# Kernel optimization log

Measured on AMD Instinct MI355X. Metric: run time of the kernel, lower is better.

## Reference

```python
import jax, jax.numpy as jnp
import numpy as np

NUM_HEADS = 12
HEAD_DIM = 64
HIDDEN = NUM_HEADS * HEAD_DIM
SCALE = 1.0 / float(np.sqrt(HEAD_DIM))


def _split_heads(x):
    # x: [b, d, s, hidden] -> [b, h, d, s, head_dim]  (transpose_for_scores)
    b, d, s, _ = x.shape
    return jnp.transpose(x.reshape(b, d, s, NUM_HEADS, HEAD_DIM), (0, 3, 1, 2, 4))


def _merge_heads(x):
    # [b, h, d, s, e] -> [b, d, s, hidden]  (untranspose_for_scores)
    b, h, d, s, e = x.shape
    return jnp.transpose(x, (0, 2, 3, 1, 4)).reshape(b, d, s, h * e)


def _segment_attention(q, keys, values, masks, num_docs):
    # _cat_forward: broadcast every key/value/mask list entry to num_docs along
    # dim 2, concat along key length, then scaled-dot-product attention.
    b, h = q.shape[0], q.shape[1]
    q = jnp.broadcast_to(q, (b, h, num_docs, q.shape[3], q.shape[4]))
    k = jnp.concatenate([jnp.broadcast_to(t, (b, h, num_docs, t.shape[3], t.shape[4])) for t in keys], axis=3)
    v = jnp.concatenate([jnp.broadcast_to(t, (b, h, num_docs, t.shape[3], t.shape[4])) for t in values], axis=3)
    mask = jnp.concatenate([jnp.broadcast_to(m, (b, 1, num_docs, 1, m.shape[-1])) for m in masks], axis=-1)
    scores = jnp.einsum('bhdqe,bhdke->bhdqk', q, k) * SCALE + mask
    probs = jax.nn.softmax(scores, axis=-1)
    ctx = jnp.einsum('bhdqk,bhdke->bhdqe', probs, v)
    return _merge_heads(ctx)


def setup_inputs() -> dict:
    key = jax.random.key(0)
    ks = jax.random.split(key, 8)
    B, D, Q, S = 2, 16, 32, 512
    inp = {
        'cls': jax.random.normal(ks[0], (B, 1, 1, HIDDEN), jnp.float32),
        'query': jax.random.normal(ks[1], (B, 1, Q, HIDDEN), jnp.float32),
        'doc': jax.random.normal(ks[2], (B, D, S, HIDDEN), jnp.float32),
        'qmask': jnp.zeros((B, 1, 1, 1, Q), jnp.float32),
        'dmask': jnp.zeros((B, 1, D, 1, S), jnp.float32),
        'Wq': jax.random.normal(ks[3], (HIDDEN, HIDDEN), jnp.float32) * 0.02,
        'bq': jnp.zeros((HIDDEN,), jnp.float32),
        'Wk': jax.random.normal(ks[4], (HIDDEN, HIDDEN), jnp.float32) * 0.02,
        'bk': jnp.zeros((HIDDEN,), jnp.float32),
        'Wv': jax.random.normal(ks[5], (HIDDEN, HIDDEN), jnp.float32) * 0.02,
        'bv': jnp.zeros((HIDDEN,), jnp.float32),
    }
    return inp


def reference(cls, query, doc, qmask, dmask, Wq, bq, Wk, bk, Wv, bv):
    num_docs = doc.shape[1]
    b = cls.shape[0]
    # per-segment q/k/v projections + head split
    segs = {}
    for name, hs in (('cls', cls), ('query', query), ('doc', doc)):
        segs[name] = tuple(_split_heads(hs @ W.T + bb) for W, bb in ((Wq, bq), (Wk, bk), (Wv, bv)))
    cmask = jnp.zeros((b, 1, 1, 1, cls.shape[2]), cls.dtype)  # cls token never padded
    masks = {'cls': cmask, 'query': qmask, 'doc': dmask}
    names = ('cls', 'query', 'doc')
    keys = [segs[n][1] for n in names]
    vals = [segs[n][2] for n in names]
    mlist = [masks[n] for n in names]
    # all segment->segment attention flags default True; attention_window_size
    # is None so each segment goes through the _cat_forward path
    outs = [_segment_attention(segs[n][0], keys, vals, mlist, num_docs) for n in names]
    # cls:[b,D,1,H], query:[b,D,Q,H], doc:[b,D,S,H] -> concat along seq for one output
    return jnp.concatenate(outs, axis=2)
```

## Files before the change

kernel.cpp:

```cpp
#include <hip/hip_runtime.h>
#include <hip/hip_bf16.h>

#define NH      12
#define HD      64
#define HID     768
#define B_      2
#define D_      16
#define QL      32
#define SL      512
#define SEQ     545
#define RPB     8225
#define TOT_ROWS 16450
#define PAD_ROWS 16512
#define VT_R    8256
#define WSZ     589824
#define SCALE_  0.125f
#define LOG2E   1.4426950408889634f
#define QSF     0.18033688011112042f

typedef __attribute__((ext_vector_type(8))) short short8;
typedef __attribute__((ext_vector_type(4))) short short4v;
typedef __attribute__((ext_vector_type(4))) float float4v;
typedef __attribute__((ext_vector_type(2))) unsigned int uint2v;

__device__ __forceinline__ short f2bf(float f) {
    __hip_bfloat16 h = __float2bfloat16(f);
    short s; __builtin_memcpy(&s, &h, 2);
    return s;
}

__device__ __forceinline__ unsigned int cvtpk(float a, float b) {
    unsigned int r;
    asm("v_cvt_pk_bf16_f32 %0, %1, %2" : "=v"(r) : "v"(a), "v"(b));
    return r;
}

__device__ __forceinline__ void gl2lds16(const short* g, short* l) {
    __builtin_amdgcn_global_load_lds(
        (const __attribute__((address_space(1))) void*)g,
        (__attribute__((address_space(3))) void*)l, 16, 0, 0);
}

#define PACK_BLKS  12384
#define WPACK_BLKS 1728

__global__ __launch_bounds__(256) void pack_all(
    const float* __restrict__ cls, const float* __restrict__ query,
    const float* __restrict__ doc,
    const float* __restrict__ Wq, const float* __restrict__ Wk,
    const float* __restrict__ Wv,
    short* __restrict__ X, short* __restrict__ Wb)
{
    int bid = blockIdx.x;
    if (bid < PACK_BLKS) {
        int idx = (bid * 256 + threadIdx.x) * 4;
        int row = idx / HID;
        int col = idx - row * HID;
        float4 v = make_float4(0.f, 0.f, 0.f, 0.f);
        if (row < TOT_ROWS) {
            int b = row / RPB;
            int r = row - b * RPB;
            const float* src;
            if (r == 0)        src = cls   + b * HID + col;
            else if (r < 33)   src = query + ((size_t)(b * QL + (r - 1))) * HID + col;
            else               src = doc   + ((size_t)(b * (D_ * SL) + (r - 33))) * HID + col;
            v = *reinterpret_cast<const float4*>(src);
        }
        short4v o;
        o[0] = f2bf(v.x); o[1] = f2bf(v.y); o[2] = f2bf(v.z); o[3] = f2bf(v.w);
        *reinterpret_cast<short4v*>(X + idx) = o;
    } else {
        int idx = ((bid - PACK_BLKS) * 256 + threadIdx.x) * 4;
        int z = idx / WSZ;
        int r = idx - z * WSZ;
        const float* src = (z == 0 ? Wq : (z == 1 ? Wk : Wv)) + r;
        float sc = (z == 0) ? QSF : 1.0f;
        float4 v = *reinterpret_cast<const float4*>(src);
        short4v o;
        o[0] = f2bf(v.x * sc); o[1] = f2bf(v.y * sc);
        o[2] = f2bf(v.z * sc); o[3] = f2bf(v.w * sc);
        *reinterpret_cast<short4v*>(Wb + idx) = o;
    }
}

__global__ __launch_bounds__(256) void proj4u(
    const short* __restrict__ X, const short* __restrict__ Wb,
    const float* __restrict__ bq, const float* __restrict__ bk,
    const float* __restrict__ bv,
    short* __restrict__ Qb, short* __restrict__ Kb, short* __restrict__ Vt)
{
    __shared__ short Xs[2][128 * 64];
    __shared__ short Ws[2][128 * 64];

    int tid = threadIdx.x, lane = tid & 63, wave = tid >> 6;

    int lin = blockIdx.x + 18 * blockIdx.y;
    {
        const int q = 290, r = 2;
        int xcd = lin & 7, seq = lin >> 3;
        lin = (xcd < r ? xcd * (q + 1) : r * (q + 1) + (xcd - r) * q) + seq;
    }
    int mblk = lin / 18;
    int nz   = lin - mblk * 18;
    int zi   = nz % 3;
    int nblk = nz / 3;
    bool vsw = (zi == 2);
    const short* W = Wb + (size_t)zi * WSZ;
    int m0 = mblk * 128, n0 = nblk * 128;

    int moff = (wave & 1) * 64, noff = (wave >> 1) * 64;
    int lr = lane & 15, lg = lane >> 4;

    const short* xsrc[4];
    const short* wsrc[4];
#pragma unroll
    for (int p = 0; p < 4; ++p) {
        int s = p * 256 + tid;
        int row = s >> 3, c = s & 7;
        int col = (c ^ (row & 7)) * 8;
        xsrc[p] = X + (size_t)(m0 + row) * HID + col;
        wsrc[p] = W + (size_t)(n0 + row) * HID + col;
    }

    float4v acc[4][4];
    for (int mi = 0; mi < 4; ++mi)
        for (int ni = 0; ni < 4; ++ni)
            acc[mi][ni] = (float4v){0.f, 0.f, 0.f, 0.f};

#define PSTAGE(bufi, kt) do {                                               \
    _Pragma("unroll")                                                       \
    for (int p = 0; p < 4; ++p) {                                           \
        gl2lds16(xsrc[p] + (kt) * 64,                                       \
                 &Xs[bufi][(p * 256 + (tid & 0xC0)) * 8]);                  \
        gl2lds16(wsrc[p] + (kt) * 64,                                       \
                 &Ws[bufi][(p * 256 + (tid & 0xC0)) * 8]);                  \
    } } while (0)

    PSTAGE(0, 0);
#pragma unroll
    for (int kt = 0; kt < 12; ++kt) {
        __syncthreads();
        if (kt < 11) PSTAGE((kt + 1) & 1, kt + 1);
        const short* xb = Xs[kt & 1];
        const short* wb = Ws[kt & 1];
        short8 afl[4], afh[4], bfl[4], bfh[4];
        for (int mi = 0; mi < 4; ++mi) {
            int r = moff + mi * 16 + lr;
            int x0 = lg ^ (r & 7);
            afl[mi] = *reinterpret_cast<const short8*>(&xb[r * 64 + x0 * 8]);
            afh[mi] = *reinterpret_cast<const short8*>(&xb[r * 64 + (x0 ^ 4) * 8]);
        }
        for (int ni = 0; ni < 4; ++ni) {
            int r = noff + ni * 16 + lr;
            int x0 = lg ^ (r & 7);
            bfl[ni] = *reinterpret_cast<const short8*>(&wb[r * 64 + x0 * 8]);
            bfh[ni] = *reinterpret_cast<const short8*>(&wb[r * 64 + (x0 ^ 4) * 8]);
        }
        if (!vsw) {
            for (int mi = 0; mi < 4; ++mi)
                for (int ni = 0; ni < 4; ++ni) {
                    acc[mi][ni] = __builtin_amdgcn_mfma_f32_16x16x32_bf16(
                        afl[mi], bfl[ni], acc[mi][ni], 0, 0, 0);
                    acc[mi][ni] = __builtin_amdgcn_mfma_f32_16x16x32_bf16(
                        afh[mi], bfh[ni], acc[mi][ni], 0, 0, 0);
                }
        } else {
            for (int mi = 0; mi < 4; ++mi)
                for (int ni = 0; ni < 4; ++ni) {
                    acc[mi][ni] = __builtin_amdgcn_mfma_f32_16x16x32_bf16(
                        bfl[ni], afl[mi], acc[mi][ni], 0, 0, 0);
                    acc[mi][ni] = __builtin_amdgcn_mfma_f32_16x16x32_bf16(
                        bfh[ni], afh[mi], acc[mi][ni], 0, 0, 0);
                }
        }
    }
#undef PSTAGE

    if (!vsw) {
        short* Y = zi == 0 ? Qb : Kb;
        const float* bias = zi == 0 ? bq : bk;
        float bsc = zi == 0 ? QSF : 1.0f;
        for (int ni = 0; ni < 4; ++ni) {
            int gcol = n0 + noff + ni * 16 + lr;
            float bb = bias[gcol] * bsc;
            for (int mi = 0; mi < 4; ++mi) {
                int growb = m0 + moff + mi * 16 + lg * 4;
                for (int r = 0; r < 4; ++r)
                    Y[(size_t)(growb + r) * HID + gcol] = f2bf(acc[mi][ni][r] + bb);
            }
        }
    } else {
        for (int ni = 0; ni < 4; ++ni) {
            float4 b4 = *reinterpret_cast<const float4*>(&bv[n0 + noff + ni * 16 + lg * 4]);
            const float* bbr = reinterpret_cast<const float*>(&b4);
            for (int mi = 0; mi < 4; ++mi) {
                int grow = m0 + moff + mi * 16 + lr;
                if (grow >= TOT_ROWS) continue;
                int b  = grow >= RPB ? 1 : 0;
                int rb = grow - b * RPB;
                int vr = rb < 33 ? rb : rb + 7;
                size_t cb = ((size_t)(b * HID + n0 + noff + ni * 16 + lg * 4)) * VT_R;
                for (int r = 0; r < 4; ++r)
                    Vt[cb + (size_t)r * VT_R + vr] = f2bf(acc[mi][ni][r] + bbr[r]);
            }
        }
    }
}

__global__ __launch_bounds__(256) void attn5(
    const short* __restrict__ Qb, const short* __restrict__ Kb,
    const short* __restrict__ Vt,
    const float* __restrict__ qmask, const float* __restrict__ dmask,
    float* __restrict__ out)
{
    __shared__ short Ks[3][64 * 64];
    __shared__ short Vs[3][64 * 64];
    __shared__ float maskv[576];

    int tid  = threadIdx.x;
    int lane = tid & 63, wave = tid >> 6;

    int lin = blockIdx.x + 3 * blockIdx.y;
    {
        int xcd = lin & 7, seq = lin >> 3;
        lin = xcd * 144 + seq;
    }
    int hbd = lin / 3;
    int qc  = lin - hbd * 3;
    int h = hbd >> 5, bd = hbd & 31;
    int b = bd >> 4, d = bd & 15;

    int lr = lane & 15, lg = lane >> 4, lk = lg * 8;
    int base = b * RPB;
    const short* vbase = Vt + (size_t)(b * HID + h * HD) * VT_R;

    const short* kp[2]; const short* vp[2];
    const short* kp8[2]; const short* vp8[2];
    int loff[2];
#pragma unroll
    for (int p = 0; p < 2; ++p) {
        int s2 = p * 256 + tid;
        int r = s2 >> 3, c = s2 & 7;
        int colsw = (c ^ (r & 7)) * 8;
        kp[p] = Kb + (size_t)(base + 33 + d * SL + r) * HID + h * HD + colsw;
        vp[p] = vbase + (size_t)r * VT_R + 40 + d * SL + colsw;
        int r8 = r > 32 ? 32 : r;
        kp8[p] = Kb + (size_t)(base + r8) * HID + h * HD + colsw;
        vp8[p] = vbase + (size_t)r * VT_R + colsw;
        loff[p] = (p * 256 + (tid & 0xC0)) * 8;
    }

#define ALIN(bufi, kt) do {                                       \
    gl2lds16(kp[0] + (size_t)(kt) * 64 * HID, &Ks[bufi][loff[0]]);\
    gl2lds16(kp[1] + (size_t)(kt) * 64 * HID, &Ks[bufi][loff[1]]);\
    gl2lds16(vp[0] + (kt) * 64, &Vs[bufi][loff[0]]);              \
    gl2lds16(vp[1] + (kt) * 64, &Vs[bufi][loff[1]]); } while (0)
#define A8(bufi) do {                                             \
    gl2lds16(kp8[0], &Ks[bufi][loff[0]]);                         \
    gl2lds16(kp8[1], &Ks[bufi][loff[1]]);                         \
    gl2lds16(vp8[0], &Vs[bufi][loff[0]]);                         \
    gl2lds16(vp8[1], &Vs[bufi][loff[1]]); } while (0)

    ALIN(0, 0);
    ALIN(1, 1);

    for (int i = tid; i < 576; i += 256) {
        float mv;
        if (i < 512)       mv = dmask[(size_t)(b * D_ + d) * SL + i];
        else if (i == 512) mv = 0.f;
        else if (i < 545)  mv = qmask[b * QL + (i - 513)];
        else               mv = -INFINITY;
        maskv[i] = mv * LOG2E;
    }

    short8 bq0[3], bq1[3];
#pragma unroll
    for (int s = 0; s < 3; ++s) {
        int qtok = qc * 192 + s * 64 + wave * 16 + lr;
        int qrow = qtok < 512 ? base + 33 + d * SL + qtok : base + qtok - 512;
        const short* qp = Qb + (size_t)qrow * HID + h * HD + lk;
        bq0[s] = *reinterpret_cast<const short8*>(qp);
        bq1[s] = *reinterpret_cast<const short8*>(qp + 32);
    }

    float m_i[3] = {-1e30f, -1e30f, -1e30f};
    float lp[3]  = {0.f, 0.f, 0.f};
    float4v o[3][4];
    for (int s = 0; s < 3; ++s)
        for (int nt = 0; nt < 4; ++nt) o[s][nt] = (float4v){0.f, 0.f, 0.f, 0.f};

    __syncthreads();

#pragma unroll
    for (int kt = 0; kt < 9; ++kt) {
        if (kt >= 1) {
            if (kt == 8) { asm volatile("s_waitcnt vmcnt(0)" ::: "memory"); }
            else         { asm volatile("s_waitcnt vmcnt(4)" ::: "memory"); }
            __builtin_amdgcn_s_barrier();
            __builtin_amdgcn_sched_barrier(0);
        }
        if (kt < 6)       ALIN((kt + 2) % 3, kt + 2);
        else if (kt == 6) A8((kt + 2) % 3);

        const short* kb   = Ks[kt % 3];
        const short* vbuf = Vs[kt % 3];

        float4v mk[4];
        short8 kf0[4], kf1[4];
#pragma unroll
        for (int nt = 0; nt < 4; ++nt) {
            mk[nt] = *reinterpret_cast<const float4v*>(
                &maskv[kt * 64 + nt * 16 + lg * 4]);
            int r = nt * 16 + lr;
            int x0 = lg ^ (r & 7);
            kf0[nt] = *reinterpret_cast<const short8*>(&kb[r * 64 + x0 * 8]);
            kf1[nt] = *reinterpret_cast<const short8*>(&kb[r * 64 + (x0 ^ 4) * 8]);
        }

#pragma unroll
        for (int s = 0; s < 3; ++s) {
            float p4[4][4];
            __builtin_amdgcn_s_setprio(1);
            for (int nt = 0; nt < 4; ++nt) {
                float4v z = mk[nt];
                z = __builtin_amdgcn_mfma_f32_16x16x32_bf16(kf0[nt], bq0[s], z, 0, 0, 0);
                z = __builtin_amdgcn_mfma_f32_16x16x32_bf16(kf1[nt], bq1[s], z, 0, 0, 0);
                for (int r = 0; r < 4; ++r) p4[nt][r] = z[r];
            }
            __builtin_amdgcn_s_setprio(0);

            float c0 = fmaxf(fmaxf(p4[0][0], p4[0][1]), p4[0][2]);
            float c1 = fmaxf(fmaxf(p4[0][3], p4[1][0]), p4[1][1]);
            float c2 = fmaxf(fmaxf(p4[1][2], p4[1][3]), p4[2][0]);
            float c3 = fmaxf(fmaxf(p4[2][1], p4[2][2]), p4[2][3]);
            float c4 = fmaxf(fmaxf(p4[3][0], p4[3][1]), p4[3][2]);
            float lmax = fmaxf(fmaxf(fmaxf(c0, c1), fmaxf(c2, c3)),
                               fmaxf(c4, p4[3][3]));

            if (__any(lmax > m_i[s] + 8.0f)) {
                float tmx = fmaxf(lmax, __shfl_xor(lmax, 16));
                tmx = fmaxf(tmx, __shfl_xor(tmx, 32));
                float mnew = fmaxf(m_i[s], tmx);
                float alpha = exp2f(m_i[s] - mnew);
                m_i[s] = mnew;
                lp[s] *= alpha;
                float al[4];
                for (int r = 0; r < 4; ++r) al[r] = __shfl(alpha, lg * 4 + r);
                for (int nt = 0; nt < 4; ++nt)
                    for (int r = 0; r < 4; ++r) o[s][nt][r] *= al[r];
            }

            for (int nt = 0; nt < 4; ++nt)
                for (int r = 0; r < 4; ++r)
                    p4[nt][r] = exp2f(p4[nt][r] - m_i[s]);
            float s0 = (p4[0][0] + p4[0][1]) + (p4[0][2] + p4[0][3]);
            float s1 = (p4[1][0] + p4[1][1]) + (p4[1][2] + p4[1][3]);
            float s2 = (p4[2][0] + p4[2][1]) + (p4[2][2] + p4[2][3]);
            float s3 = (p4[3][0] + p4[3][1]) + (p4[3][2] + p4[3][3]);
            lp[s] += (s0 + s1) + (s2 + s3);

            unsigned int wa[4], wbv[4];
            for (int nt = 0; nt < 4; ++nt) {
                wa[nt]  = cvtpk(p4[nt][0], p4[nt][1]);
                wbv[nt] = cvtpk(p4[nt][2], p4[nt][3]);
            }
            uint2v tA01 = __builtin_amdgcn_permlane32_swap(wa[0],  wa[1],  false, false);
            uint2v uA01 = __builtin_amdgcn_permlane16_swap(tA01[0], tA01[1], false, false);
            uint2v tB01 = __builtin_amdgcn_permlane32_swap(wbv[0], wbv[1], false, false);
            uint2v uB01 = __builtin_amdgcn_permlane16_swap(tB01[0], tB01[1], false, false);
            uint2v tA23 = __builtin_amdgcn_permlane32_swap(wa[2],  wa[3],  false, false);
            uint2v uA23 = __builtin_amdgcn_permlane16_swap(tA23[0], tA23[1], false, false);
            uint2v tB23 = __builtin_amdgcn_permlane32_swap(wbv[2], wbv[3], false, false);
            uint2v uB23 = __builtin_amdgcn_permlane16_swap(tB23[0], tB23[1], false, false);

            union { unsigned int u[4]; short8 s8; } A0, A1;
            A0.u[0] = uA01[0]; A0.u[1] = uB01[0]; A0.u[2] = uA01[1]; A0.u[3] = uB01[1];
            A1.u[0] = uA23[0]; A1.u[1] = uB23[0]; A1.u[2] = uA23[1]; A1.u[3] = uB23[1];
            short8 ap0 = A0.s8;
            short8 ap1 = A1.s8;

            __builtin_amdgcn_s_setprio(1);
            for (int nt = 0; nt < 4; ++nt) {
                int rd = nt * 16 + lr;
                int x0 = lg ^ (rd & 7);
                short8 bv0 = *reinterpret_cast<const short8*>(&vbuf[rd * 64 + x0 * 8]);
                short8 bv1 = *reinterpret_cast<const short8*>(&vbuf[rd * 64 + (x0 ^ 4) * 8]);
                o[s][nt] = __builtin_amdgcn_mfma_f32_16x16x32_bf16(ap0, bv0, o[s][nt], 0, 0, 0);
                o[s][nt] = __builtin_amdgcn_mfma_f32_16x16x32_bf16(ap1, bv1, o[s][nt], 0, 0, 0);
            }
            __builtin_amdgcn_s_setprio(0);
        }
    }
#undef ALIN
#undef A8

    for (int s = 0; s < 3; ++s) {
        float lt = lp[s];
        lt += __shfl_xor(lt, 16);
        lt += __shfl_xor(lt, 32);
        float li[4];
        for (int r = 0; r < 4; ++r) li[r] = __shfl(lt, lg * 4 + r);
        for (int r = 0; r < 4; ++r) {
            int t = qc * 192 + s * 64 + wave * 16 + lg * 4 + r;
            if (t >= SEQ) continue;
            int seq = t < 512 ? 33 + t : (t == 512 ? 0 : t - 512);
            float inv = 1.f / li[r];
            float* op = out + ((size_t)(bd * SEQ + seq)) * HID + h * HD + lr;
            for (int nt = 0; nt < 4; ++nt)
                op[nt * 16] = o[s][nt][r] * inv;
        }
    }
}

extern "C" void kernel_launch(void* const* d_in, const int* in_sizes, int n_in,
                              void* d_out, int out_size, void* d_ws, size_t ws_size,
                              hipStream_t stream)
{
    const float* cls   = (const float*)d_in[0];
    const float* query = (const float*)d_in[1];
    const float* doc   = (const float*)d_in[2];
    const float* qmask = (const float*)d_in[3];
    const float* dmask = (const float*)d_in[4];
    const float* Wq = (const float*)d_in[5];
    const float* bq = (const float*)d_in[6];
    const float* Wk = (const float*)d_in[7];
    const float* bk = (const float*)d_in[8];
    const float* Wv = (const float*)d_in[9];
    const float* bv = (const float*)d_in[10];
    float* out = (float*)d_out;

    short* X  = (short*)d_ws;
    size_t seg = (size_t)PAD_ROWS * HID;
    short* Qb = X + seg;
    short* Kb = Qb + seg;
    short* Vt = Kb + seg;
    short* Wb = (short*)d_out;

    pack_all<<<dim3(PACK_BLKS + WPACK_BLKS), 256, 0, stream>>>(
        cls, query, doc, Wq, Wk, Wv, X, Wb);
    proj4u<<<dim3(18, 129, 1), 256, 0, stream>>>(X, Wb, bq, bk, bv, Qb, Kb, Vt);
    attn5<<<dim3(3, NH * 32, 1), 256, 0, stream>>>(Qb, Kb, Vt, qmask, dmask, out);
}
```

Baseline: 278.3 us.

## Split attention query sub-tiles across 12 waves instead of looping in 4

```diff
diff --git a/kernel.cpp b/kernel.cpp
--- a/kernel.cpp
+++ b/kernel.cpp
@@ -207,7 +207,7 @@
     }
 }
 
-__global__ __launch_bounds__(256) void attn5(
+__global__ __launch_bounds__(768) void attn6(
     const short* __restrict__ Qb, const short* __restrict__ Kb,
     const short* __restrict__ Vt,
     const float* __restrict__ qmask, const float* __restrict__ dmask,
@@ -231,40 +231,37 @@
     int b = bd >> 4, d = bd & 15;
 
     int lr = lane & 15, lg = lane >> 4, lk = lg * 8;
+    int sidx = wave >> 2, wq = wave & 3;
     int base = b * RPB;
     const short* vbase = Vt + (size_t)(b * HID + h * HD) * VT_R;
 
-    const short* kp[2]; const short* vp[2];
-    const short* kp8[2]; const short* vp8[2];
-    int loff[2];
-#pragma unroll
-    for (int p = 0; p < 2; ++p) {
-        int s2 = p * 256 + tid;
-        int r = s2 >> 3, c = s2 & 7;
+    bool stg = tid < 512;
+    int loffK = (tid & 0x1C0) * 8;
+    const short *kp = Kb, *vp = Vt, *kp8 = Kb, *vp8 = Vt;
+    {
+        int r = tid >> 3, c = tid & 7;
         int colsw = (c ^ (r & 7)) * 8;
-        kp[p] = Kb + (size_t)(base + 33 + d * SL + r) * HID + h * HD + colsw;
-        vp[p] = vbase + (size_t)r * VT_R + 40 + d * SL + colsw;
-        int r8 = r > 32 ? 32 : r;
-        kp8[p] = Kb + (size_t)(base + r8) * HID + h * HD + colsw;
-        vp8[p] = vbase + (size_t)r * VT_R + colsw;
-        loff[p] = (p * 256 + (tid & 0xC0)) * 8;
-    }
-
-#define ALIN(bufi, kt) do {                                       \
-    gl2lds16(kp[0] + (size_t)(kt) * 64 * HID, &Ks[bufi][loff[0]]);\
-    gl2lds16(kp[1] + (size_t)(kt) * 64 * HID, &Ks[bufi][loff[1]]);\
-    gl2lds16(vp[0] + (kt) * 64, &Vs[bufi][loff[0]]);              \
-    gl2lds16(vp[1] + (kt) * 64, &Vs[bufi][loff[1]]); } while (0)
-#define A8(bufi) do {                                             \
-    gl2lds16(kp8[0], &Ks[bufi][loff[0]]);                         \
-    gl2lds16(kp8[1], &Ks[bufi][loff[1]]);                         \
-    gl2lds16(vp8[0], &Vs[bufi][loff[0]]);                         \
-    gl2lds16(vp8[1], &Vs[bufi][loff[1]]); } while (0)
+        if (stg) {
+            kp  = Kb + (size_t)(base + 33 + d * SL + r) * HID + h * HD + colsw;
+            vp  = vbase + (size_t)r * VT_R + 40 + d * SL + colsw;
+            int r8 = r > 32 ? 32 : r;
+            kp8 = Kb + (size_t)(base + r8) * HID + h * HD + colsw;
+            vp8 = vbase + (size_t)r * VT_R + colsw;
+        }
+    }
+
+#define ALIN(bufi, kt) do { if (stg) {                            \
+    gl2lds16(kp + (size_t)(kt) * 64 * HID, &Ks[bufi][loffK]);     \
+    gl2lds16(vp + (kt) * 64, &Vs[bufi][loffK]); } } while (0)
+#define A8(bufi) do { if (stg) {                                  \
+    gl2lds16(kp8, &Ks[bufi][loffK]);                              \
+    gl2lds16(vp8, &Vs[bufi][loffK]); } } while (0)
 
     ALIN(0, 0);
     ALIN(1, 1);
 
-    for (int i = tid; i < 576; i += 256) {
+    if (tid < 576) {
+        int i = tid;
         float mv;
         if (i < 512)       mv = dmask[(size_t)(b * D_ + d) * SL + i];
         else if (i == 512) mv = 0.f;
@@ -273,21 +270,19 @@
         maskv[i] = mv * LOG2E;
     }
 
-    short8 bq0[3], bq1[3];
-#pragma unroll
-    for (int s = 0; s < 3; ++s) {
-        int qtok = qc * 192 + s * 64 + wave * 16 + lr;
+    short8 bq0, bq1;
+    {
+        int qtok = qc * 192 + sidx * 64 + wq * 16 + lr;
         int qrow = qtok < 512 ? base + 33 + d * SL + qtok : base + qtok - 512;
         const short* qp = Qb + (size_t)qrow * HID + h * HD + lk;
-        bq0[s] = *reinterpret_cast<const short8*>(qp);
-        bq1[s] = *reinterpret_cast<const short8*>(qp + 32);
-    }
-
-    float m_i[3] = {-1e30f, -1e30f, -1e30f};
-    float lp[3]  = {0.f, 0.f, 0.f};
-    float4v o[3][4];
-    for (int s = 0; s < 3; ++s)
-        for (int nt = 0; nt < 4; ++nt) o[s][nt] = (float4v){0.f, 0.f, 0.f, 0.f};
+        bq0 = *reinterpret_cast<const short8*>(qp);
+        bq1 = *reinterpret_cast<const short8*>(qp + 32);
+    }
+
+    float m_i = -1e30f;
+    float lp  = 0.f;
+    float4v o[4];
+    for (int nt = 0; nt < 4; ++nt) o[nt] = (float4v){0.f, 0.f, 0.f, 0.f};
 
     __syncthreads();
 
@@ -295,7 +290,7 @@
     for (int kt = 0; kt < 9; ++kt) {
         if (kt >= 1) {
             if (kt == 8) { asm volatile("s_waitcnt vmcnt(0)" ::: "memory"); }
-            else         { asm volatile("s_waitcnt vmcnt(4)" ::: "memory"); }
+            else         { asm volatile("s_waitcnt vmcnt(2)" ::: "memory"); }
             __builtin_amdgcn_s_barrier();
             __builtin_amdgcn_sched_barrier(0);
         }
@@ -305,109 +300,105 @@
         const short* kb   = Ks[kt % 3];
         const short* vbuf = Vs[kt % 3];
 
-        float4v mk[4];
+        float p4[4][4];
         short8 kf0[4], kf1[4];
 #pragma unroll
         for (int nt = 0; nt < 4; ++nt) {
-            mk[nt] = *reinterpret_cast<const float4v*>(
-                &maskv[kt * 64 + nt * 16 + lg * 4]);
             int r = nt * 16 + lr;
             int x0 = lg ^ (r & 7);
             kf0[nt] = *reinterpret_cast<const short8*>(&kb[r * 64 + x0 * 8]);
             kf1[nt] = *reinterpret_cast<const short8*>(&kb[r * 64 + (x0 ^ 4) * 8]);
         }
-
-#pragma unroll
-        for (int s = 0; s < 3; ++s) {
-            float p4[4][4];
-            __builtin_amdgcn_s_setprio(1);
-            for (int nt = 0; nt < 4; ++nt) {
-                float4v z = mk[nt];
-                z = __builtin_amdgcn_mfma_f32_16x16x32_bf16(kf0[nt], bq0[s], z, 0, 0, 0);
-                z = __builtin_amdgcn_mfma_f32_16x16x32_bf16(kf1[nt], bq1[s], z, 0, 0, 0);
-                for (int r = 0; r < 4; ++r) p4[nt][r] = z[r];
-            }
-            __builtin_amdgcn_s_setprio(0);
-
-            float c0 = fmaxf(fmaxf(p4[0][0], p4[0][1]), p4[0][2]);
-            float c1 = fmaxf(fmaxf(p4[0][3], p4[1][0]), p4[1][1]);
-            float c2 = fmaxf(fmaxf(p4[1][2], p4[1][3]), p4[2][0]);
-            float c3 = fmaxf(fmaxf(p4[2][1], p4[2][2]), p4[2][3]);
-            float c4 = fmaxf(fmaxf(p4[3][0], p4[3][1]), p4[3][2]);
-            float lmax = fmaxf(fmaxf(fmaxf(c0, c1), fmaxf(c2, c3)),
-                               fmaxf(c4, p4[3][3]));
-
-            if (__any(lmax > m_i[s] + 8.0f)) {
-                float tmx = fmaxf(lmax, __shfl_xor(lmax, 16));
-                tmx = fmaxf(tmx, __shfl_xor(tmx, 32));
-                float mnew = fmaxf(m_i[s], tmx);
-                float alpha = exp2f(m_i[s] - mnew);
-                m_i[s] = mnew;
-                lp[s] *= alpha;
-                float al[4];
-                for (int r = 0; r < 4; ++r) al[r] = __shfl(alpha, lg * 4 + r);
-                for (int nt = 0; nt < 4; ++nt)
-                    for (int r = 0; r < 4; ++r) o[s][nt][r] *= al[r];
-            }
-
+        __builtin_amdgcn_s_setprio(1);
+#pragma unroll
+        for (int nt = 0; nt < 4; ++nt) {
+            float4v z = *reinterpret_cast<const float4v*>(
+                &maskv[kt * 64 + nt * 16 + lg * 4]);
+            z = __builtin_amdgcn_mfma_f32_16x16x32_bf16(kf0[nt], bq0, z, 0, 0, 0);
+            z = __builtin_amdgcn_mfma_f32_16x16x32_bf16(kf1[nt], bq1, z, 0, 0, 0);
+            for (int r = 0; r < 4; ++r) p4[nt][r] = z[r];
+        }
+        __builtin_amdgcn_s_setprio(0);
+
+        float c0 = fmaxf(fmaxf(p4[0][0], p4[0][1]), p4[0][2]);
+        float c1 = fmaxf(fmaxf(p4[0][3], p4[1][0]), p4[1][1]);
+        float c2 = fmaxf(fmaxf(p4[1][2], p4[1][3]), p4[2][0]);
+        float c3 = fmaxf(fmaxf(p4[2][1], p4[2][2]), p4[2][3]);
+        float c4 = fmaxf(fmaxf(p4[3][0], p4[3][1]), p4[3][2]);
+        float lmax = fmaxf(fmaxf(fmaxf(c0, c1), fmaxf(c2, c3)),
+                           fmaxf(c4, p4[3][3]));
+
+        if (__any(lmax > m_i + 8.0f)) {
+            float tmx = fmaxf(lmax, __shfl_xor(lmax, 16));
+            tmx = fmaxf(tmx, __shfl_xor(tmx, 32));
+            float mnew = fmaxf(m_i, tmx);
+            float alpha = exp2f(m_i - mnew);
+            m_i = mnew;
+            lp *= alpha;
+            float al[4];
+            for (int r = 0; r < 4; ++r) al[r] = __shfl(alpha, lg * 4 + r);
             for (int nt = 0; nt < 4; ++nt)
-                for (int r = 0; r < 4; ++r)
-                    p4[nt][r] = exp2f(p4[nt][r] - m_i[s]);
-            float s0 = (p4[0][0] + p4[0][1]) + (p4[0][2] + p4[0][3]);
-            float s1 = (p4[1][0] + p4[1][1]) + (p4[1][2] + p4[1][3]);
-            float s2 = (p4[2][0] + p4[2][1]) + (p4[2][2] + p4[2][3]);
-            float s3 = (p4[3][0] + p4[3][1]) + (p4[3][2] + p4[3][3]);
-            lp[s] += (s0 + s1) + (s2 + s3);
-
-            unsigned int wa[4], wbv[4];
-            for (int nt = 0; nt < 4; ++nt) {
-                wa[nt]  = cvtpk(p4[nt][0], p4[nt][1]);
-                wbv[nt] = cvtpk(p4[nt][2], p4[nt][3]);
-            }
-            uint2v tA01 = __builtin_amdgcn_permlane32_swap(wa[0],  wa[1],  false, false);
-            uint2v uA01 = __builtin_amdgcn_permlane16_swap(tA01[0], tA01[1], false, false);
-            uint2v tB01 = __builtin_amdgcn_permlane32_swap(wbv[0], wbv[1], false, false);
-            uint2v uB01 = __builtin_amdgcn_permlane16_swap(tB01[0], tB01[1], false, false);
-            uint2v tA23 = __builtin_amdgcn_permlane32_swap(wa[2],  wa[3],  false, false);
-            uint2v uA23 = __builtin_amdgcn_permlane16_swap(tA23[0], tA23[1], false, false);
-            uint2v tB23 = __builtin_amdgcn_permlane32_swap(wbv[2], wbv[3], false, false);
-            uint2v uB23 = __builtin_amdgcn_permlane16_swap(tB23[0], tB23[1], false, false);
-
-            union { unsigned int u[4]; short8 s8; } A0, A1;
-            A0.u[0] = uA01[0]; A0.u[1] = uB01[0]; A0.u[2] = uA01[1]; A0.u[3] = uB01[1];
-            A1.u[0] = uA23[0]; A1.u[1] = uB23[0]; A1.u[2] = uA23[1]; A1.u[3] = uB23[1];
-            short8 ap0 = A0.s8;
-            short8 ap1 = A1.s8;
-
-            __builtin_amdgcn_s_setprio(1);
-            for (int nt = 0; nt < 4; ++nt) {
-                int rd = nt * 16 + lr;
-                int x0 = lg ^ (rd & 7);
-                short8 bv0 = *reinterpret_cast<const short8*>(&vbuf[rd * 64 + x0 * 8]);
-                short8 bv1 = *reinterpret_cast<const short8*>(&vbuf[rd * 64 + (x0 ^ 4) * 8]);
-                o[s][nt] = __builtin_amdgcn_mfma_f32_16x16x32_bf16(ap0, bv0, o[s][nt], 0, 0, 0);
-                o[s][nt] = __builtin_amdgcn_mfma_f32_16x16x32_bf16(ap1, bv1, o[s][nt], 0, 0, 0);
-            }
-            __builtin_amdgcn_s_setprio(0);
-        }
+                for (int r = 0; r < 4; ++r) o[nt][r] *= al[r];
+        }
+
+        for (int nt = 0; nt < 4; ++nt)
+            for (int r = 0; r < 4; ++r)
+                p4[nt][r] = exp2f(p4[nt][r] - m_i);
+        float s0 = (p4[0][0] + p4[0][1]) + (p4[0][2] + p4[0][3]);
+        float s1 = (p4[1][0] + p4[1][1]) + (p4[1][2] + p4[1][3]);
+        float s2 = (p4[2][0] + p4[2][1]) + (p4[2][2] + p4[2][3]);
+        float s3 = (p4[3][0] + p4[3][1]) + (p4[3][2] + p4[3][3]);
+        lp += (s0 + s1) + (s2 + s3);
+
+        unsigned int wa[4], wbv[4];
+        for (int nt = 0; nt < 4; ++nt) {
+            wa[nt]  = cvtpk(p4[nt][0], p4[nt][1]);
+            wbv[nt] = cvtpk(p4[nt][2], p4[nt][3]);
+        }
+        uint2v tA01 = __builtin_amdgcn_permlane32_swap(wa[0],  wa[1],  false, false);
+        uint2v uA01 = __builtin_amdgcn_permlane16_swap(tA01[0], tA01[1], false, false);
+        uint2v tB01 = __builtin_amdgcn_permlane32_swap(wbv[0], wbv[1], false, false);
+        uint2v uB01 = __builtin_amdgcn_permlane16_swap(tB01[0], tB01[1], false, false);
+        uint2v tA23 = __builtin_amdgcn_permlane32_swap(wa[2],  wa[3],  false, false);
+        uint2v uA23 = __builtin_amdgcn_permlane16_swap(tA23[0], tA23[1], false, false);
+        uint2v tB23 = __builtin_amdgcn_permlane32_swap(wbv[2], wbv[3], false, false);
+        uint2v uB23 = __builtin_amdgcn_permlane16_swap(tB23[0], tB23[1], false, false);
+
+        union { unsigned int u[4]; short8 s8; } A0, A1;
+        A0.u[0] = uA01[0]; A0.u[1] = uB01[0]; A0.u[2] = uA01[1]; A0.u[3] = uB01[1];
+        A1.u[0] = uA23[0]; A1.u[1] = uB23[0]; A1.u[2] = uA23[1]; A1.u[3] = uB23[1];
+        short8 ap0 = A0.s8;
+        short8 ap1 = A1.s8;
+
+        __builtin_amdgcn_s_setprio(1);
+#pragma unroll
+        for (int nt = 0; nt < 4; ++nt) {
+            int rd = nt * 16 + lr;
+            int x0 = lg ^ (rd & 7);
+            short8 bv0 = *reinterpret_cast<const short8*>(&vbuf[rd * 64 + x0 * 8]);
+            short8 bv1 = *reinterpret_cast<const short8*>(&vbuf[rd * 64 + (x0 ^ 4) * 8]);
+            o[nt] = __builtin_amdgcn_mfma_f32_16x16x32_bf16(ap0, bv0, o[nt], 0, 0, 0);
+            o[nt] = __builtin_amdgcn_mfma_f32_16x16x32_bf16(ap1, bv1, o[nt], 0, 0, 0);
+        }
+        __builtin_amdgcn_s_setprio(0);
     }
 #undef ALIN
 #undef A8
 
-    for (int s = 0; s < 3; ++s) {
-        float lt = lp[s];
+    {
+        float lt = lp;
         lt += __shfl_xor(lt, 16);
         lt += __shfl_xor(lt, 32);
         float li[4];
         for (int r = 0; r < 4; ++r) li[r] = __shfl(lt, lg * 4 + r);
         for (int r = 0; r < 4; ++r) {
-            int t = qc * 192 + s * 64 + wave * 16 + lg * 4 + r;
+            int t = qc * 192 + sidx * 64 + wq * 16 + lg * 4 + r;
             if (t >= SEQ) continue;
             int seq = t < 512 ? 33 + t : (t == 512 ? 0 : t - 512);
             float inv = 1.f / li[r];
             float* op = out + ((size_t)(bd * SEQ + seq)) * HID + h * HD + lr;
             for (int nt = 0; nt < 4; ++nt)
-                op[nt * 16] = o[s][nt][r] * inv;
+                op[nt * 16] = o[nt][r] * inv;
         }
     }
 }
@@ -439,5 +430,5 @@
     pack_all<<<dim3(PACK_BLKS + WPACK_BLKS), 256, 0, stream>>>(
         cls, query, doc, Wq, Wk, Wv, X, Wb);
     proj4u<<<dim3(18, 129, 1), 256, 0, stream>>>(X, Wb, bq, bk, bv, Qb, Kb, Vt);
-    attn5<<<dim3(3, NH * 32, 1), 256, 0, stream>>>(Qb, Kb, Vt, qmask, dmask, out);
-}
+    attn6<<<dim3(3, NH * 32, 1), 768, 0, stream>>>(Qb, Kb, Vt, qmask, dmask, out);
+}
```

Result: faster. 270.5 us (-2.8%).
